# Optimization experiments

Measured on AMD Instinct MI355X. Metric: run time of the kernel, lower is better.

Reference implementation:

```python
import jax, jax.numpy as jnp
import numpy as np

HEAD_DIM = 64
NUM_Q_HEADS = 32
NUM_KV_HEADS = 4
ROPE_THETA = 10000.0


def setup_inputs() -> dict:
    key = jax.random.key(0)
    k1, k2, k3 = jax.random.split(key, 3)
    b, s, h = 1, 2048, 2048
    qkv_out = (NUM_Q_HEADS + 2 * NUM_KV_HEADS) * HEAD_DIM  # 2560
    return {
        "hidden_states": jax.random.normal(k1, (b, s, h), dtype=jnp.float32),
        "w_qkv": jax.random.normal(k2, (qkv_out, h), dtype=jnp.float32) * (h ** -0.5),
        "w_o": jax.random.normal(k3, (h, NUM_Q_HEADS * HEAD_DIM), dtype=jnp.float32) * ((NUM_Q_HEADS * HEAD_DIM) ** -0.5),
    }


def _apply_rope(x, cos, sin):
    # x: (b, s, h, d); cos/sin: (s, d//2)
    d2 = x.shape[-1] // 2
    x1, x2 = x[..., :d2], x[..., d2:]
    c = cos[None, :, None, :]
    sn = sin[None, :, None, :]
    return jnp.concatenate([x1 * c - x2 * sn, x2 * c + x1 * sn], axis=-1)


def reference(hidden_states, w_qkv, w_o):
    b, s, _ = hidden_states.shape
    d, h_q, h_kv = HEAD_DIM, NUM_Q_HEADS, NUM_KV_HEADS
    g = h_q // h_kv  # GQA group size

    # fused QKV projection + reshape
    qkv = jnp.einsum('bsh,oh->bso', hidden_states, w_qkv)
    qkv = qkv.reshape(b, s, h_q + 2 * h_kv, d)
    q = qkv[:, :, :h_q]
    k = qkv[:, :, h_q:h_q + h_kv]
    v = qkv[:, :, h_q + h_kv:]

    # RoPE
    pos = jnp.arange(s, dtype=jnp.float32)
    inv_freq = 1.0 / (ROPE_THETA ** (jnp.arange(0, d, 2, dtype=jnp.float32) / d))
    ang = pos[:, None] * inv_freq[None, :]  # (s, d//2)
    cos, sin = jnp.cos(ang), jnp.sin(ang)
    q = _apply_rope(q, cos, sin)
    k = _apply_rope(k, cos, sin)

    # GQA causal attention
    qh = q.transpose(0, 2, 1, 3).reshape(b, h_kv, g, s, d)
    kh = k.transpose(0, 2, 1, 3)  # (b, h_kv, s, d)
    vh = v.transpose(0, 2, 1, 3)
    scale = d ** -0.5
    scores = jnp.einsum('bhgqd,bhkd->bhgqk', qh, kh) * scale
    causal = jnp.tril(jnp.ones((s, s), dtype=bool))
    scores = jnp.where(causal[None, None, None], scores, jnp.finfo(scores.dtype).min)
    attn = jax.nn.softmax(scores, axis=-1)
    out = jnp.einsum('bhgqk,bhkd->bhgqd', attn, vh)
    out = out.reshape(b, h_q, s, d).transpose(0, 2, 1, 3).reshape(b, s, h_q * d)

    return jnp.einsum('bse,he->bsh', out, w_o)
```

## Files before the change

kernel.cpp:

```cpp
#include <hip/hip_runtime.h>
#include <stdint.h>

#define SEQ 2048
#define HQ 32
#define HKV 4
#define DH 64

typedef __attribute__((ext_vector_type(8))) short bf16x8;
typedef __attribute__((ext_vector_type(4))) float f32x4;

static __device__ __forceinline__ unsigned short f2bf(float f) {
  unsigned int u = __builtin_bit_cast(unsigned int, f);
  u += 0x7fffu + ((u >> 16) & 1u);
  return (unsigned short)(u >> 16);
}

static __device__ __forceinline__ void gload_lds16(const void* g, void* l) {
  __builtin_amdgcn_global_load_lds((const __attribute__((address_space(1))) void*)g,
                                   (__attribute__((address_space(3))) void*)l,
                                   16, 0, 0);
}

__global__ __launch_bounds__(256) void cvt_kernel(const float* __restrict__ in,
                                                  unsigned short* __restrict__ out, int n) {
  int i = (blockIdx.x * 256 + threadIdx.x) * 4;
  if (i < n) {
    float4 v = *(const float4*)(in + i);
    ushort4 o;
    o.x = f2bf(v.x);
    o.y = f2bf(v.y);
    o.z = f2bf(v.z);
    o.w = f2bf(v.w);
    *(ushort4*)(out + i) = o;
  }
}

__global__ __launch_bounds__(256) void rope_tab_kernel(float2* __restrict__ tab) {
  int idx = blockIdx.x * 256 + threadIdx.x;
  int i = idx & 31;
  int s = idx >> 5;
  float ang = (float)s * exp2f((float)i * (-0.41524101186092029f));
  tab[idx] = make_float2(cosf(ang), sinf(ang));
}

__global__ __launch_bounds__(256) void gemm_bt_kernel(const unsigned short* __restrict__ A,
                                                      const unsigned short* __restrict__ B,
                                                      float* __restrict__ C,
                                                      int M, int N, int K) {
  __shared__ __align__(16) unsigned short Al[2][128][32];
  __shared__ __align__(16) unsigned short Bl[2][128][32];
  const int t = threadIdx.x;
  const int lane = t & 63;
  const int w = t >> 6;
  const int wr = w >> 1, wc = w & 1;
  const int l15 = lane & 15, l4 = lane >> 4;
  const long bm = (long)blockIdx.y * 128;
  const long bn = (long)blockIdx.x * 128;

  const unsigned short* ga0 = A + (bm + w * 32 + (lane >> 2)) * (long)K + (lane & 3) * 8;
  const unsigned short* ga1 = ga0 + 16 * (long)K;
  const unsigned short* gb0 = B + (bn + w * 32 + (lane >> 2)) * (long)K + (lane & 3) * 8;
  const unsigned short* gb1 = gb0 + 16 * (long)K;

  auto STAGE = [&](int buf, int k0) {
    gload_lds16(ga0 + k0, &Al[buf][w * 32][0]);
    gload_lds16(ga1 + k0, &Al[buf][w * 32 + 16][0]);
    gload_lds16(gb0 + k0, &Bl[buf][w * 32][0]);
    gload_lds16(gb1 + k0, &Bl[buf][w * 32 + 16][0]);
  };

  f32x4 acc[4][4] = {};

  STAGE(0, 0);
  __syncthreads();
  int cur = 0;
  for (int k0 = 0; k0 < K; k0 += 32) {
    if (k0 + 32 < K) STAGE(cur ^ 1, k0 + 32);

    bf16x8 af[4], bfr[4];
#pragma unroll
    for (int mi = 0; mi < 4; mi++)
      af[mi] = *(const bf16x8*)&Al[cur][wr * 64 + mi * 16 + l15][l4 * 8];
#pragma unroll
    for (int ni = 0; ni < 4; ni++)
      bfr[ni] = *(const bf16x8*)&Bl[cur][wc * 64 + ni * 16 + l15][l4 * 8];
#pragma unroll
    for (int mi = 0; mi < 4; mi++)
#pragma unroll
      for (int ni = 0; ni < 4; ni++)
        acc[mi][ni] = __builtin_amdgcn_mfma_f32_16x16x32_bf16(af[mi], bfr[ni], acc[mi][ni], 0, 0, 0);
    __syncthreads();
    cur ^= 1;
  }

#pragma unroll
  for (int mi = 0; mi < 4; mi++)
#pragma unroll
    for (int ni = 0; ni < 4; ni++)
#pragma unroll
      for (int j = 0; j < 4; j++) {
        long row = bm + wr * 64 + mi * 16 + l4 * 4 + j;
        long col = bn + wc * 64 + ni * 16 + l15;
        C[row * (long)N + col] = acc[mi][ni][j];
      }
}

__global__ __launch_bounds__(256) void gemm_qkv_rope_kernel(const unsigned short* __restrict__ A,
                                                            const unsigned short* __restrict__ B,
                                                            const float2* __restrict__ tab,
                                                            unsigned short* __restrict__ q,
                                                            unsigned short* __restrict__ k,
                                                            unsigned short* __restrict__ vf) {
  __shared__ __align__(16) unsigned short Al[2][128][32];
  __shared__ __align__(16) unsigned short Bl[2][128][32];
  const int K = 2048;
  const int t = threadIdx.x;
  const int lane = t & 63;
  const int w = t >> 6;
  const int wr = w >> 1, wc = w & 1;
  const int l15 = lane & 15, l4 = lane >> 4;
  const long bm = (long)blockIdx.y * 128;
  const long bn = (long)blockIdx.x * 128;

  const unsigned short* ga0 = A + (bm + w * 32 + (lane >> 2)) * (long)K + (lane & 3) * 8;
  const unsigned short* ga1 = ga0 + 16 * (long)K;
  const unsigned short* gb0 = B + (bn + w * 32 + (lane >> 2)) * (long)K + (lane & 3) * 8;
  const unsigned short* gb1 = gb0 + 16 * (long)K;

  auto STAGE = [&](int buf, int k0) {
    gload_lds16(ga0 + k0, &Al[buf][w * 32][0]);
    gload_lds16(ga1 + k0, &Al[buf][w * 32 + 16][0]);
    gload_lds16(gb0 + k0, &Bl[buf][w * 32][0]);
    gload_lds16(gb1 + k0, &Bl[buf][w * 32 + 16][0]);
  };

  f32x4 acc[4][4] = {};

  STAGE(0, 0);
  __syncthreads();
  int cur = 0;
  for (int k0 = 0; k0 < K; k0 += 32) {
    if (k0 + 32 < K) STAGE(cur ^ 1, k0 + 32);

    bf16x8 af[4], bfr[4];
#pragma unroll
    for (int mi = 0; mi < 4; mi++)
      af[mi] = *(const bf16x8*)&Al[cur][wr * 64 + mi * 16 + l15][l4 * 8];
#pragma unroll
    for (int ni = 0; ni < 4; ni++)
      bfr[ni] = *(const bf16x8*)&Bl[cur][wc * 64 + ni * 16 + l15][l4 * 8];
#pragma unroll
    for (int mi = 0; mi < 4; mi++)
#pragma unroll
      for (int ni = 0; ni < 4; ni++)
        acc[mi][ni] = __builtin_amdgcn_mfma_f32_16x16x32_bf16(af[mi], bfr[ni], acc[mi][ni], 0, 0, 0);
    __syncthreads();
    cur ^= 1;
  }

  const int hh = (int)(bn >> 6) + wc;
  if (hh < 32) {
    unsigned short* base = q + (long)hh * SEQ * 64;
#pragma unroll
    for (int mi = 0; mi < 4; mi++)
#pragma unroll
      for (int j = 0; j < 4; j++) {
        long s = bm + wr * 64 + mi * 16 + l4 * 4 + j;
#pragma unroll
        for (int ni = 0; ni < 2; ni++) {
          int i = ni * 16 + l15;
          float2 cs = tab[s * 32 + i];
          float x1 = acc[mi][ni][j];
          float x2 = acc[mi][ni + 2][j];
          base[s * 64 + i] = f2bf((x1 * cs.x - x2 * cs.y) * 0.125f);
          base[s * 64 + i + 32] = f2bf((x2 * cs.x + x1 * cs.y) * 0.125f);
        }
      }
  } else if (hh < 36) {
    unsigned short* base = k + (long)(hh - 32) * SEQ * 64;
#pragma unroll
    for (int mi = 0; mi < 4; mi++)
#pragma unroll
      for (int j = 0; j < 4; j++) {
        long s = bm + wr * 64 + mi * 16 + l4 * 4 + j;
        long t8 = (s >> 6) * 4096;
        int n_ = (int)((s >> 4) & 3);
        int sl = (int)(s & 15);
#pragma unroll
        for (int ni = 0; ni < 2; ni++) {
          int i = ni * 16 + l15;
          float2 cs = tab[s * 32 + i];
          float x1 = acc[mi][ni][j];
          float x2 = acc[mi][ni + 2][j];
          long sub = ((i >> 3) * 16 + sl) * 8 + (i & 7);
          base[t8 + n_ * 512 + sub] = f2bf(x1 * cs.x - x2 * cs.y);
          base[t8 + (4 + n_) * 512 + sub] = f2bf(x2 * cs.x + x1 * cs.y);
        }
      }
  } else {
    unsigned short* base = vf + (long)(hh - 36) * SEQ * 64;
#pragma unroll
    for (int mi = 0; mi < 4; mi++)
#pragma unroll
      for (int j = 0; j < 4; j++) {
        long s = bm + wr * 64 + mi * 16 + l4 * 4 + j;
        long t8 = (s >> 6) * 4096;
        int kc = (int)((s >> 5) & 1);
        int l4s = (int)((s >> 3) & 3);
        int jj = (int)(s & 7);
#pragma unroll
        for (int ni = 0; ni < 4; ni++) {
          base[t8 + ((kc * 4 + ni) * 64 + l4s * 16 + l15) * 8 + jj] = f2bf(acc[mi][ni][j]);
        }
      }
  }
}

__global__ __launch_bounds__(512) void attn_kernel(const unsigned short* __restrict__ Q,
                                                   const unsigned short* __restrict__ KF,
                                                   const unsigned short* __restrict__ VF,
                                                   unsigned short* __restrict__ O) {
  const int h = blockIdx.x;
  const int qt = 15 - blockIdx.y;
  const int kvh = h >> 3;
  const int t = threadIdx.x;
  const int lane = t & 63;
  const int w = t >> 6;
  const int l15 = lane & 15, l4 = lane >> 4;

  __shared__ __align__(16) unsigned short Kl[2][4096];
  __shared__ __align__(16) unsigned short Vl[2][4096];
  __shared__ __align__(16) unsigned short P[8][16][72];

  const int qrow0 = qt * 128 + w * 16;
  const unsigned short* qb = Q + ((long)h * SEQ + qrow0) * 64;
  bf16x8 qf[2];
  qf[0] = *(const bf16x8*)(qb + (long)l15 * 64 + l4 * 8);
  qf[1] = *(const bf16x8*)(qb + (long)l15 * 64 + 32 + l4 * 8);

  const unsigned short* kbg = KF + (long)kvh * SEQ * 64;
  const unsigned short* vbg = VF + (long)kvh * SEQ * 64;

  f32x4 acc_o[4] = {};
  f32x4 l_part = {};

  const int steps = 2 * qt + 2;

  auto STAGE = [&](int buf, int tile) {
    gload_lds16(kbg + (long)tile * 4096 + w * 512 + lane * 8, &Kl[buf][w * 512]);
    gload_lds16(vbg + (long)tile * 4096 + w * 512 + lane * 8, &Vl[buf][w * 512]);
  };

  STAGE(0, 0);
  __syncthreads();
  int buf = 0;
  for (int tt = 0; tt < steps; tt++) {
    if (tt + 1 < steps) STAGE(buf ^ 1, tt + 1);

    f32x4 sacc[4] = {};
#pragma unroll
    for (int c = 0; c < 2; c++) {
      bf16x8 kf[4];
#pragma unroll
      for (int n = 0; n < 4; n++)
        kf[n] = *(const bf16x8*)&Kl[buf][(c * 4 + n) * 512 + lane * 8];
#pragma unroll
      for (int n = 0; n < 4; n++)
        sacc[n] = __builtin_amdgcn_mfma_f32_16x16x32_bf16(qf[c], kf[n], sacc[n], 0, 0, 0);
    }

    const int kv0 = tt * 64;
#pragma unroll
    for (int j = 0; j < 4; j++) {
      int qrow = qrow0 + l4 * 4 + j;
      float p[4];
#pragma unroll
      for (int n = 0; n < 4; n++) {
        float pv = __expf(sacc[n][j]);
        p[n] = (kv0 + n * 16 + l15 <= qrow) ? pv : 0.0f;
      }
      l_part[j] += (p[0] + p[1]) + (p[2] + p[3]);
#pragma unroll
      for (int n = 0; n < 4; n++)
        P[w][l4 * 4 + j][n * 16 + l15] = f2bf(p[n]);
    }

#pragma unroll
    for (int kc = 0; kc < 2; kc++) {
      bf16x8 pf = *(const bf16x8*)&P[w][l15][kc * 32 + l4 * 8];
      bf16x8 vfr[4];
#pragma unroll
      for (int ni = 0; ni < 4; ni++)
        vfr[ni] = *(const bf16x8*)&Vl[buf][(kc * 4 + ni) * 512 + lane * 8];
#pragma unroll
      for (int ni = 0; ni < 4; ni++)
        acc_o[ni] = __builtin_amdgcn_mfma_f32_16x16x32_bf16(pf, vfr[ni], acc_o[ni], 0, 0, 0);
    }

    __syncthreads();
    buf ^= 1;
  }

  f32x4 inv;
#pragma unroll
  for (int j = 0; j < 4; j++) {
    float rs = l_part[j];
#pragma unroll
    for (int msk = 1; msk < 16; msk <<= 1) rs += __shfl_xor(rs, msk);
    inv[j] = 1.0f / rs;
  }
#pragma unroll
  for (int ni = 0; ni < 4; ni++)
#pragma unroll
    for (int j = 0; j < 4; j++) {
      long row = (long)qrow0 + l4 * 4 + j;
      O[row * (HQ * 64) + h * 64 + ni * 16 + l15] = f2bf(acc_o[ni][j] * inv[j]);
    }
}

extern "C" void kernel_launch(void* const* d_in, const int* in_sizes, int n_in,
                              void* d_out, int out_size, void* d_ws, size_t ws_size,
                              hipStream_t stream) {
  const float* hidden = (const float*)d_in[0];
  const float* w_qkv = (const float*)d_in[1];
  const float* w_o = (const float*)d_in[2];
  float* out = (float*)d_out;
  char* ws = (char*)d_ws;

  unsigned short* hs_bf   = (unsigned short*)(ws + 0);
  unsigned short* wqkv_bf = (unsigned short*)(ws + 8388608);
  unsigned short* wo_bf   = (unsigned short*)(ws + 18874368);
  unsigned short* q_bf    = (unsigned short*)(ws + 27262976);
  unsigned short* kf_bf   = (unsigned short*)(ws + 35651584);
  unsigned short* vf_bf   = (unsigned short*)(ws + 36700160);
  unsigned short* attn_bf = (unsigned short*)(ws + 37748736);
  float2*         tab     = (float2*)(ws + 46137344);

  cvt_kernel<<<4096, 256, 0, stream>>>(hidden, hs_bf, 2048 * 2048);
  cvt_kernel<<<5120, 256, 0, stream>>>(w_qkv, wqkv_bf, 2560 * 2048);
  cvt_kernel<<<4096, 256, 0, stream>>>(w_o, wo_bf, 2048 * 2048);
  rope_tab_kernel<<<256, 256, 0, stream>>>(tab);

  gemm_qkv_rope_kernel<<<dim3(20, 16), 256, 0, stream>>>(hs_bf, wqkv_bf, tab, q_bf, kf_bf, vf_bf);

  attn_kernel<<<dim3(32, 16), 512, 0, stream>>>(q_bf, kf_bf, vf_bf, attn_bf);

  gemm_bt_kernel<<<dim3(16, 16), 256, 0, stream>>>(attn_bf, wo_bf, out, 2048, 2048, 2048);
}
```

Measured before the change: 231.9 us.

## Halve GEMM M-tile to 64 rows and merge conversion/RoPE-table launches

Both GEMMs now use 64x128 output tiles instead of 128x128. Staging goes through one combined LDS buffer of 192 rows, loaded by three 16-row chunks per wave. This doubles the grid from 320 and 256 blocks to 640 and 512, so the 256 CUs are better filled and per-thread accumulator registers drop. The cost is lower operand reuse per block and more global/L2 traffic. Separately, the three fp32-to-bf16 conversions and the RoPE table build are merged into one launch to cut kernel launch overhead.

```diff
diff --git a/kernel.cpp b/kernel.cpp
--- a/kernel.cpp
+++ b/kernel.cpp
@@ -21,10 +21,22 @@
                                    16, 0, 0);
 }
 
-__global__ __launch_bounds__(256) void cvt_kernel(const float* __restrict__ in,
-                                                  unsigned short* __restrict__ out, int n) {
-  int i = (blockIdx.x * 256 + threadIdx.x) * 4;
-  if (i < n) {
+__global__ __launch_bounds__(256) void cvtall_kernel(const float* __restrict__ hidden,
+                                                     const float* __restrict__ w_qkv,
+                                                     const float* __restrict__ w_o,
+                                                     unsigned short* __restrict__ hs_bf,
+                                                     unsigned short* __restrict__ wqkv_bf,
+                                                     unsigned short* __restrict__ wo_bf,
+                                                     float2* __restrict__ tab) {
+  int b = blockIdx.x;
+  if (b < 13312) {
+    const float* in;
+    unsigned short* out;
+    int off;
+    if (b < 4096) { in = hidden; out = hs_bf; off = b; }
+    else if (b < 9216) { in = w_qkv; out = wqkv_bf; off = b - 4096; }
+    else { in = w_o; out = wo_bf; off = b - 9216; }
+    int i = (off * 256 + threadIdx.x) * 4;
     float4 v = *(const float4*)(in + i);
     ushort4 o;
     o.x = f2bf(v.x);
@@ -32,44 +44,44 @@
     o.z = f2bf(v.z);
     o.w = f2bf(v.w);
     *(ushort4*)(out + i) = o;
-  }
-}
-
-__global__ __launch_bounds__(256) void rope_tab_kernel(float2* __restrict__ tab) {
-  int idx = blockIdx.x * 256 + threadIdx.x;
-  int i = idx & 31;
-  int s = idx >> 5;
-  float ang = (float)s * exp2f((float)i * (-0.41524101186092029f));
-  tab[idx] = make_float2(cosf(ang), sinf(ang));
+  } else {
+    int idx = (b - 13312) * 256 + threadIdx.x;
+    int i = idx & 31;
+    int s = idx >> 5;
+    float ang = (float)s * exp2f((float)i * (-0.41524101186092029f));
+    tab[idx] = make_float2(cosf(ang), sinf(ang));
+  }
 }
 
 __global__ __launch_bounds__(256) void gemm_bt_kernel(const unsigned short* __restrict__ A,
                                                       const unsigned short* __restrict__ B,
                                                       float* __restrict__ C,
                                                       int M, int N, int K) {
-  __shared__ __align__(16) unsigned short Al[2][128][32];
-  __shared__ __align__(16) unsigned short Bl[2][128][32];
+  __shared__ __align__(16) unsigned short Tl[2][192 * 32];
   const int t = threadIdx.x;
   const int lane = t & 63;
   const int w = t >> 6;
   const int wr = w >> 1, wc = w & 1;
   const int l15 = lane & 15, l4 = lane >> 4;
-  const long bm = (long)blockIdx.y * 128;
+  const long bm = (long)blockIdx.y * 64;
   const long bn = (long)blockIdx.x * 128;
 
-  const unsigned short* ga0 = A + (bm + w * 32 + (lane >> 2)) * (long)K + (lane & 3) * 8;
-  const unsigned short* ga1 = ga0 + 16 * (long)K;
-  const unsigned short* gb0 = B + (bn + w * 32 + (lane >> 2)) * (long)K + (lane & 3) * 8;
-  const unsigned short* gb1 = gb0 + 16 * (long)K;
+  const unsigned short* gsrc[3];
+#pragma unroll
+  for (int i = 0; i < 3; i++) {
+    int c = w * 3 + i;
+    long row = (c < 4) ? (bm + c * 16) : (bn + (c - 4) * 16);
+    const unsigned short* gp = (c < 4) ? A : B;
+    gsrc[i] = gp + (row + (lane >> 2)) * (long)K + (lane & 3) * 8;
+  }
 
   auto STAGE = [&](int buf, int k0) {
-    gload_lds16(ga0 + k0, &Al[buf][w * 32][0]);
-    gload_lds16(ga1 + k0, &Al[buf][w * 32 + 16][0]);
-    gload_lds16(gb0 + k0, &Bl[buf][w * 32][0]);
-    gload_lds16(gb1 + k0, &Bl[buf][w * 32 + 16][0]);
+#pragma unroll
+    for (int i = 0; i < 3; i++)
+      gload_lds16(gsrc[i] + k0, &Tl[buf][(w * 3 + i) * 512]);
   };
 
-  f32x4 acc[4][4] = {};
+  f32x4 acc[2][4] = {};
 
   STAGE(0, 0);
   __syncthreads();
@@ -77,15 +89,15 @@
   for (int k0 = 0; k0 < K; k0 += 32) {
     if (k0 + 32 < K) STAGE(cur ^ 1, k0 + 32);
 
-    bf16x8 af[4], bfr[4];
-#pragma unroll
-    for (int mi = 0; mi < 4; mi++)
-      af[mi] = *(const bf16x8*)&Al[cur][wr * 64 + mi * 16 + l15][l4 * 8];
+    bf16x8 af[2], bfr[4];
+#pragma unroll
+    for (int mi = 0; mi < 2; mi++)
+      af[mi] = *(const bf16x8*)&Tl[cur][(wr * 32 + mi * 16 + l15) * 32 + l4 * 8];
 #pragma unroll
     for (int ni = 0; ni < 4; ni++)
-      bfr[ni] = *(const bf16x8*)&Bl[cur][wc * 64 + ni * 16 + l15][l4 * 8];
-#pragma unroll
-    for (int mi = 0; mi < 4; mi++)
+      bfr[ni] = *(const bf16x8*)&Tl[cur][(64 + wc * 64 + ni * 16 + l15) * 32 + l4 * 8];
+#pragma unroll
+    for (int mi = 0; mi < 2; mi++)
 #pragma unroll
       for (int ni = 0; ni < 4; ni++)
         acc[mi][ni] = __builtin_amdgcn_mfma_f32_16x16x32_bf16(af[mi], bfr[ni], acc[mi][ni], 0, 0, 0);
@@ -94,12 +106,12 @@
   }
 
 #pragma unroll
-  for (int mi = 0; mi < 4; mi++)
+  for (int mi = 0; mi < 2; mi++)
 #pragma unroll
     for (int ni = 0; ni < 4; ni++)
 #pragma unroll
       for (int j = 0; j < 4; j++) {
-        long row = bm + wr * 64 + mi * 16 + l4 * 4 + j;
+        long row = bm + wr * 32 + mi * 16 + l4 * 4 + j;
         long col = bn + wc * 64 + ni * 16 + l15;
         C[row * (long)N + col] = acc[mi][ni][j];
       }
@@ -111,30 +123,32 @@
                                                             unsigned short* __restrict__ q,
                                                             unsigned short* __restrict__ k,
                                                             unsigned short* __restrict__ vf) {
-  __shared__ __align__(16) unsigned short Al[2][128][32];
-  __shared__ __align__(16) unsigned short Bl[2][128][32];
+  __shared__ __align__(16) unsigned short Tl[2][192 * 32];
   const int K = 2048;
   const int t = threadIdx.x;
   const int lane = t & 63;
   const int w = t >> 6;
   const int wr = w >> 1, wc = w & 1;
   const int l15 = lane & 15, l4 = lane >> 4;
-  const long bm = (long)blockIdx.y * 128;
+  const long bm = (long)blockIdx.y * 64;
   const long bn = (long)blockIdx.x * 128;
 
-  const unsigned short* ga0 = A + (bm + w * 32 + (lane >> 2)) * (long)K + (lane & 3) * 8;
-  const unsigned short* ga1 = ga0 + 16 * (long)K;
-  const unsigned short* gb0 = B + (bn + w * 32 + (lane >> 2)) * (long)K + (lane & 3) * 8;
-  const unsigned short* gb1 = gb0 + 16 * (long)K;
+  const unsigned short* gsrc[3];
+#pragma unroll
+  for (int i = 0; i < 3; i++) {
+    int c = w * 3 + i;
+    long row = (c < 4) ? (bm + c * 16) : (bn + (c - 4) * 16);
+    const unsigned short* gp = (c < 4) ? A : B;
+    gsrc[i] = gp + (row + (lane >> 2)) * (long)K + (lane & 3) * 8;
+  }
 
   auto STAGE = [&](int buf, int k0) {
-    gload_lds16(ga0 + k0, &Al[buf][w * 32][0]);
-    gload_lds16(ga1 + k0, &Al[buf][w * 32 + 16][0]);
-    gload_lds16(gb0 + k0, &Bl[buf][w * 32][0]);
-    gload_lds16(gb1 + k0, &Bl[buf][w * 32 + 16][0]);
+#pragma unroll
+    for (int i = 0; i < 3; i++)
+      gload_lds16(gsrc[i] + k0, &Tl[buf][(w * 3 + i) * 512]);
   };
 
-  f32x4 acc[4][4] = {};
+  f32x4 acc[2][4] = {};
 
   STAGE(0, 0);
   __syncthreads();
@@ -142,15 +156,15 @@
   for (int k0 = 0; k0 < K; k0 += 32) {
     if (k0 + 32 < K) STAGE(cur ^ 1, k0 + 32);
 
-    bf16x8 af[4], bfr[4];
-#pragma unroll
-    for (int mi = 0; mi < 4; mi++)
-      af[mi] = *(const bf16x8*)&Al[cur][wr * 64 + mi * 16 + l15][l4 * 8];
+    bf16x8 af[2], bfr[4];
+#pragma unroll
+    for (int mi = 0; mi < 2; mi++)
+      af[mi] = *(const bf16x8*)&Tl[cur][(wr * 32 + mi * 16 + l15) * 32 + l4 * 8];
 #pragma unroll
     for (int ni = 0; ni < 4; ni++)
-      bfr[ni] = *(const bf16x8*)&Bl[cur][wc * 64 + ni * 16 + l15][l4 * 8];
-#pragma unroll
-    for (int mi = 0; mi < 4; mi++)
+      bfr[ni] = *(const bf16x8*)&Tl[cur][(64 + wc * 64 + ni * 16 + l15) * 32 + l4 * 8];
+#pragma unroll
+    for (int mi = 0; mi < 2; mi++)
 #pragma unroll
       for (int ni = 0; ni < 4; ni++)
         acc[mi][ni] = __builtin_amdgcn_mfma_f32_16x16x32_bf16(af[mi], bfr[ni], acc[mi][ni], 0, 0, 0);
@@ -162,10 +176,10 @@
   if (hh < 32) {
     unsigned short* base = q + (long)hh * SEQ * 64;
 #pragma unroll
-    for (int mi = 0; mi < 4; mi++)
+    for (int mi = 0; mi < 2; mi++)
 #pragma unroll
       for (int j = 0; j < 4; j++) {
-        long s = bm + wr * 64 + mi * 16 + l4 * 4 + j;
+        long s = bm + wr * 32 + mi * 16 + l4 * 4 + j;
 #pragma unroll
         for (int ni = 0; ni < 2; ni++) {
           int i = ni * 16 + l15;
@@ -179,10 +193,10 @@
   } else if (hh < 36) {
     unsigned short* base = k + (long)(hh - 32) * SEQ * 64;
 #pragma unroll
-    for (int mi = 0; mi < 4; mi++)
+    for (int mi = 0; mi < 2; mi++)
 #pragma unroll
       for (int j = 0; j < 4; j++) {
-        long s = bm + wr * 64 + mi * 16 + l4 * 4 + j;
+        long s = bm + wr * 32 + mi * 16 + l4 * 4 + j;
         long t8 = (s >> 6) * 4096;
         int n_ = (int)((s >> 4) & 3);
         int sl = (int)(s & 15);
@@ -200,10 +214,10 @@
   } else {
     unsigned short* base = vf + (long)(hh - 36) * SEQ * 64;
 #pragma unroll
-    for (int mi = 0; mi < 4; mi++)
+    for (int mi = 0; mi < 2; mi++)
 #pragma unroll
       for (int j = 0; j < 4; j++) {
-        long s = bm + wr * 64 + mi * 16 + l4 * 4 + j;
+        long s = bm + wr * 32 + mi * 16 + l4 * 4 + j;
         long t8 = (s >> 6) * 4096;
         int kc = (int)((s >> 5) & 1);
         int l4s = (int)((s >> 3) & 3);
@@ -336,14 +350,11 @@
   unsigned short* attn_bf = (unsigned short*)(ws + 37748736);
   float2*         tab     = (float2*)(ws + 46137344);
 
-  cvt_kernel<<<4096, 256, 0, stream>>>(hidden, hs_bf, 2048 * 2048);
-  cvt_kernel<<<5120, 256, 0, stream>>>(w_qkv, wqkv_bf, 2560 * 2048);
-  cvt_kernel<<<4096, 256, 0, stream>>>(w_o, wo_bf, 2048 * 2048);
-  rope_tab_kernel<<<256, 256, 0, stream>>>(tab);
-
-  gemm_qkv_rope_kernel<<<dim3(20, 16), 256, 0, stream>>>(hs_bf, wqkv_bf, tab, q_bf, kf_bf, vf_bf);
+  cvtall_kernel<<<13568, 256, 0, stream>>>(hidden, w_qkv, w_o, hs_bf, wqkv_bf, wo_bf, tab);
+
+  gemm_qkv_rope_kernel<<<dim3(20, 32), 256, 0, stream>>>(hs_bf, wqkv_bf, tab, q_bf, kf_bf, vf_bf);
 
   attn_kernel<<<dim3(32, 16), 512, 0, stream>>>(q_bf, kf_bf, vf_bf, attn_bf);
 
-  gemm_bt_kernel<<<dim3(16, 16), 256, 0, stream>>>(attn_bf, wo_bf, out, 2048, 2048, 2048);
-}
+  gemm_bt_kernel<<<dim3(16, 32), 256, 0, stream>>>(attn_bf, wo_bf, out, 2048, 2048, 2048);
+}
```

Measured after the change: 205.1 us. 11.6% less time.
